# Performance work log

Hardware: AMD Instinct MI355X
Metric: run time of the kernel (lower is better)

The kernel has to match this reference:

```python
import jax, jax.numpy as jnp
import numpy as np

D_MODEL = 1024
D_STATE = 16
EPS = 1e-5


def _layernorm(x, g, b):
    mu = x.mean(-1, keepdims=True)
    xc = x - mu
    var = (xc * xc).mean(-1, keepdims=True)
    return xc * jax.lax.rsqrt(var + EPS) * g + b


def setup_inputs() -> dict:
    key = jax.random.key(0)
    ks = jax.random.split(key, 10)
    B, L, d, n = 8, 1024, D_MODEL, D_STATE
    s = 1.0 / np.sqrt(d)
    return {
        "x": jax.random.normal(ks[0], (B, L, d), jnp.float32),
        "h_prev": jnp.zeros((B, d * n), jnp.float32),
        "ln_g": jnp.ones((d,), jnp.float32),
        "ln_b": jnp.zeros((d,), jnp.float32),
        "W_ig": jax.random.uniform(ks[1], (2 * d, d), jnp.float32, -s, s),
        "W_dt": jax.random.uniform(ks[2], (d, d), jnp.float32, -s, s),
        "b_dt": jax.random.uniform(ks[3], (d,), jnp.float32, -s, s),
        "A_log": jax.random.uniform(ks[4], (d, n), jnp.float32, -3.0, -1.0),
        "W_B": jax.random.uniform(ks[5], (n, d), jnp.float32, -s, s),
        "W_C": jax.random.uniform(ks[6], (n, d), jnp.float32, -s, s),
        "D": jnp.ones((d,), jnp.float32),
        "W_out": jax.random.uniform(ks[7], (d, d), jnp.float32, -s, s),
    }


def reference(x, h_prev, ln_g, ln_b, W_ig, W_dt, b_dt, A_log, W_B, W_C, D, W_out):
    Bsz, L, d = x.shape
    n = A_log.shape[1]
    x_norm = _layernorm(x, ln_g, ln_b)
    x_proj = jnp.einsum('bld,ed->ble', x_norm, W_ig)  # [B,L,2d]
    x_in, z = x_proj[..., :d], x_proj[..., d:]
    dt = jax.nn.softplus(jnp.einsum('bld,ed->ble', x_in, W_dt) + b_dt)  # [B,L,d]
    A = -jnp.exp(A_log)  # [d,n]
    B_t = jnp.einsum('bld,nd->bln', x_in, W_B)  # [B,L,n]
    C_t = jnp.einsum('bld,nd->bln', x_in, W_C)  # [B,L,n]
    h0 = h_prev.reshape(Bsz, d, n)

    def step(h, inp):
        dt_t, xin_t, Bt_t, Ct_t = inp  # [B,d],[B,d],[B,n],[B,n]
        dA = jnp.exp(dt_t[..., None] * A)                      # [B,d,n]
        h = dA * h + (dt_t * xin_t)[..., None] * Bt_t[:, None, :]
        y_t = (h * Ct_t[:, None, :]).sum(-1)                   # [B,d]
        return h, y_t

    xs = (jnp.swapaxes(dt, 0, 1), jnp.swapaxes(x_in, 0, 1),
          jnp.swapaxes(B_t, 0, 1), jnp.swapaxes(C_t, 0, 1))
    h_final, y = jax.lax.scan(step, h0, xs)
    y = jnp.swapaxes(y, 0, 1)  # [B,L,d]
    ssm_out = y * jax.nn.silu(z) + x_in * D
    out = jnp.einsum('bld,ed->ble', ssm_out, W_out)
    return (x + out, h_final.reshape(Bsz, -1))
```

## Files before the change

kernel.cpp:

```cpp
#include <hip/hip_runtime.h>
#include <hip/hip_bf16.h>
#include <math.h>

#define DM 1024
#define NS 16
#define BSZ 8
#define LSEQ 1024
#define MROWS (BSZ*LSEQ)
#define CH 32
#define ROWP 36

typedef __bf16 bf16;
typedef bf16 bf16x8 __attribute__((ext_vector_type(8)));
typedef bf16 bf16x4 __attribute__((ext_vector_type(4)));
typedef float f32x4 __attribute__((ext_vector_type(4)));
typedef unsigned int u32;
typedef unsigned short u16;
typedef u32 u32x4 __attribute__((ext_vector_type(4)));

__device__ __forceinline__ void async16(const void* g, void* l) {
  __builtin_amdgcn_global_load_lds((const __attribute__((address_space(1))) void*)g,
                                   (__attribute__((address_space(3))) void*)l,
                                   16, 0, 0);
}

__device__ __forceinline__ float bflo(u32 u) { return __builtin_bit_cast(float, (u32)(u << 16)); }
__device__ __forceinline__ float bfhi(u32 u) { return __builtin_bit_cast(float, (u32)(u & 0xffff0000u)); }

template <int CTRL>
__device__ __forceinline__ float dpp_shr_add(float y) {
  int s = __builtin_amdgcn_update_dpp(0, __builtin_bit_cast(int, y), CTRL, 0xf, 0xf, true);
  return y + __builtin_bit_cast(float, s);
}
__device__ __forceinline__ float row16_sum(float y) {
  y = dpp_shr_add<0x111>(y);
  y = dpp_shr_add<0x112>(y);
  y = dpp_shr_add<0x114>(y);
  y = dpp_shr_add<0x118>(y);
  return y;
}

__global__ void cast_f2b(const float* __restrict__ s, bf16* __restrict__ d, int n4) {
  int i = blockIdx.x * 256 + threadIdx.x;
  if (i < n4) {
    float4 v = ((const float4*)s)[i];
    bf16x4 o;
    o.x = (bf16)v.x; o.y = (bf16)v.y; o.z = (bf16)v.z; o.w = (bf16)v.w;
    *(bf16x4*)(d + 4 * (size_t)i) = o;
  }
}

__global__ void transpose_cast(const float* __restrict__ src, bf16* __restrict__ dst) {
  __shared__ float tile[64][65];
  const int bk = blockIdx.x * 64;
  const int bd = blockIdx.y * 64;
  const int t = threadIdx.x;
  const int c4 = t & 15;
  const int r0 = t >> 4;
#pragma unroll
  for (int p = 0; p < 4; ++p) {
    int r = r0 + p * 16;
    float4 v = *(const float4*)(src + (size_t)(bd + r) * 1024 + bk + c4 * 4);
    tile[r][c4 * 4 + 0] = v.x;
    tile[r][c4 * 4 + 1] = v.y;
    tile[r][c4 * 4 + 2] = v.z;
    tile[r][c4 * 4 + 3] = v.w;
  }
  __syncthreads();
#pragma unroll
  for (int p = 0; p < 4; ++p) {
    int r = r0 + p * 16;
    bf16x4 o;
    o.x = (bf16)tile[c4 * 4 + 0][r];
    o.y = (bf16)tile[c4 * 4 + 1][r];
    o.z = (bf16)tile[c4 * 4 + 2][r];
    o.w = (bf16)tile[c4 * 4 + 3][r];
    *(bf16x4*)(dst + (size_t)(bk + r) * 1024 + bd + c4 * 4) = o;
  }
}

__global__ void ln_kernel(const float* __restrict__ x, const float* __restrict__ g,
                          const float* __restrict__ b, bf16* __restrict__ out) {
  const size_t row = blockIdx.x;
  const int t = threadIdx.x;
  float4 v = ((const float4*)(x + row * DM))[t];
  float s = v.x + v.y + v.z + v.w;
  float s2 = v.x*v.x + v.y*v.y + v.z*v.z + v.w*v.w;
#pragma unroll
  for (int m = 1; m < 64; m <<= 1) { s += __shfl_xor(s, m, 64); s2 += __shfl_xor(s2, m, 64); }
  __shared__ float red[8];
  int wave = t >> 6, lane = t & 63;
  if (lane == 0) { red[wave] = s; red[4 + wave] = s2; }
  __syncthreads();
  s  = red[0] + red[1] + red[2] + red[3];
  s2 = red[4] + red[5] + red[6] + red[7];
  float mu  = s * (1.f / DM);
  float var = s2 * (1.f / DM) - mu * mu;
  float inv = rsqrtf(var + 1e-5f);
  float4 gg = ((const float4*)g)[t];
  float4 bb = ((const float4*)b)[t];
  bf16x4 o;
  o.x = (bf16)((v.x - mu) * inv * gg.x + bb.x);
  o.y = (bf16)((v.y - mu) * inv * gg.y + bb.y);
  o.z = (bf16)((v.z - mu) * inv * gg.z + bb.z);
  o.w = (bf16)((v.w - mu) * inv * gg.w + bb.w);
  *(bf16x4*)(out + row * DM + t * 4) = o;
}

template <int EPI, bool SWZ>
__global__ __launch_bounds__(256)
void gemm_bf16(const bf16* __restrict__ A, const bf16* __restrict__ W, int K,
               float* __restrict__ out_f, bf16* __restrict__ out_b,
               u16* __restrict__ out_u1, u16* __restrict__ out_u2,
               const float* __restrict__ aux,
               float* __restrict__ out_f3, float* __restrict__ out_f4) {
  __shared__ bf16 As[3][128 * 32];
  __shared__ bf16 Bs[3][128 * 32];
  int tx, ty;
  if (SWZ) {
    int g = blockIdx.x;
    int xcd = g & 7, slot = g >> 3;
    tx = slot >> 3;
    ty = xcd * 8 + (slot & 7);
  } else {
    tx = blockIdx.x; ty = blockIdx.y;
  }
  const int tid  = threadIdx.x;
  const int wave = tid >> 6, lane = tid & 63;
  const int lr = lane & 15, quad = lane >> 4;
  const size_t arow = (size_t)ty * 128;
  const size_t brow = (size_t)tx * 128;
  f32x4 acc[4][4] = {};

  const int srl  = lane >> 2;
  const int kg   = lane & 3;
  const int srow = wave * 32 + srl;
  const int skc  = (kg ^ ((srl >> 1) & 3)) * 8;
  const bf16* ag = A + (arow + srow) * (size_t)K + skc;
  const bf16* wg = W + (brow + srow) * (size_t)K + skc;

  const int soff = wave * 32 * 32;
  const int ra   = (((wave >> 1) * 64) + lr) * 32 + ((quad ^ ((lr >> 1) & 3)) * 8);
  const int rb   = (((wave & 1)  * 64) + lr) * 32 + ((quad ^ ((lr >> 1) & 3)) * 8);

  bf16 *aw0 = &As[0][soff], *aw1 = &As[1][soff], *aw2 = &As[2][soff];
  bf16 *bw0 = &Bs[0][soff], *bw1 = &Bs[1][soff], *bw2 = &Bs[2][soff];
  const bf16 *ar0 = &As[0][ra], *ar1 = &As[1][ra], *ar2 = &As[2][ra];
  const bf16 *br0 = &Bs[0][rb], *br1 = &Bs[1][rb], *br2 = &Bs[2][rb];

  auto STAGE = [&](bf16* adst, bf16* bdst, int kk) {
    async16(ag + kk,                       adst);
    async16(ag + (size_t)16 * K + kk,      adst + 16 * 32);
    async16(wg + kk,                       bdst);
    async16(wg + (size_t)16 * K + kk,      bdst + 16 * 32);
  };
  auto COMPUTE = [&](const bf16* ap, const bf16* bp) {
    bf16x8 af[4], bfr[4];
#pragma unroll
    for (int i = 0; i < 4; ++i) af[i] = *(const bf16x8*)(ap + i * 16 * 32);
#pragma unroll
    for (int j = 0; j < 4; ++j) bfr[j] = *(const bf16x8*)(bp + j * 16 * 32);
#pragma unroll
    for (int i = 0; i < 4; ++i)
#pragma unroll
      for (int j = 0; j < 4; ++j)
        acc[i][j] = __builtin_amdgcn_mfma_f32_16x16x32_bf16(af[i], bfr[j], acc[i][j], 0, 0, 0);
  };

  STAGE(aw0, bw0, 0);
  STAGE(aw1, bw1, 32);
  asm volatile("s_waitcnt vmcnt(4)" ::: "memory");
  __builtin_amdgcn_s_barrier();

  for (int k0 = 0; k0 < K; k0 += 32) {
    const bool pf = (k0 + 64 < K);
    if (pf) STAGE(aw2, bw2, k0 + 64);
    COMPUTE(ar0, br0);
    if (pf) asm volatile("s_waitcnt vmcnt(4)" ::: "memory");
    else    asm volatile("s_waitcnt vmcnt(0)" ::: "memory");
    __builtin_amdgcn_s_barrier();
    bf16* t0;
    t0 = aw0; aw0 = aw1; aw1 = aw2; aw2 = t0;
    t0 = bw0; bw0 = bw1; bw1 = bw2; bw2 = t0;
    const bf16* t1;
    t1 = ar0; ar0 = ar1; ar1 = ar2; ar2 = t1;
    t1 = br0; br0 = br1; br1 = br2; br2 = t1;
  }

  const size_t mbase = arow + (wave >> 1) * 64;
  const size_t nbase = brow + (wave & 1) * 64;
  if (EPI == 0) {
    if (nbase < DM) {
#pragma unroll
      for (int i = 0; i < 4; ++i)
#pragma unroll
        for (int j = 0; j < 4; ++j)
#pragma unroll
          for (int r = 0; r < 4; ++r) {
            size_t m = mbase + i * 16 + quad * 4 + r;
            size_t n = nbase + j * 16 + lr;
            out_u1[m * DM + n] = __builtin_bit_cast(u16, (bf16)acc[i][j][r]);
          }
    } else if (nbase < 2 * DM) {
#pragma unroll
      for (int i = 0; i < 4; ++i)
#pragma unroll
        for (int j = 0; j < 4; ++j)
#pragma unroll
          for (int r = 0; r < 4; ++r) {
            size_t m = mbase + i * 16 + quad * 4 + r;
            size_t n = nbase - DM + j * 16 + lr;
            out_b[m * DM + n] = (bf16)acc[i][j][r];
          }
    } else if (nbase < 3 * DM) {
#pragma unroll
      for (int i = 0; i < 4; ++i)
#pragma unroll
        for (int j = 0; j < 4; ++j)
#pragma unroll
          for (int r = 0; r < 4; ++r) {
            size_t m = mbase + i * 16 + quad * 4 + r;
            size_t n = nbase - 2 * DM + j * 16 + lr;
            float tt = acc[i][j][r] + aux[n];
            float sp = (tt > 20.f) ? tt : __logf(1.f + __expf(tt));
            out_u2[m * DM + n] = __builtin_bit_cast(u16, (bf16)sp);
          }
    } else if (nbase < 3 * DM + 2 * NS) {
#pragma unroll
      for (int i = 0; i < 4; ++i)
#pragma unroll
        for (int r = 0; r < 4; ++r) {
          size_t m = mbase + i * 16 + quad * 4 + r;
          out_f3[m * NS + lr] = acc[i][0][r];
          out_f4[m * NS + lr] = acc[i][1][r];
        }
    }
  } else {
#pragma unroll
    for (int i = 0; i < 4; ++i)
#pragma unroll
      for (int j = 0; j < 4; ++j)
#pragma unroll
        for (int r = 0; r < 4; ++r) {
          size_t m = mbase + i * 16 + quad * 4 + r;
          size_t n = nbase + j * 16 + lr;
          float v = acc[i][j][r];
          if (EPI == 2) {
            out_f[m * DM + n] = v + aux[m * DM + n];
          } else {
            out_b[m * (size_t)DM + n] = (bf16)v;
          }
        }
  }
}

__global__ __launch_bounds__(256)
void scan_kernel(const u16* __restrict__ dt_b, const u16* __restrict__ xi_b,
                 const bf16* __restrict__ z_b,
                 const float* __restrict__ B_t, const float* __restrict__ C_t,
                 const float* __restrict__ A_log, const float* __restrict__ h_prev,
                 const float* __restrict__ Dvec,
                 bf16* __restrict__ ssm_out, float* __restrict__ h_final) {
  const int blk = blockIdx.x;
  const int b = blk >> 6;
  const int d0 = (blk & 63) * 16;
  const int t = threadIdx.x;
  const int n = t & 15, dl = t >> 4;
  const int d = d0 + dl;
  const float Ac2 = -__expf(A_log[d * NS + n]) * 1.44269504f;
  float h = h_prev[(size_t)b * DM * NS + (size_t)d * NS + n];

  __shared__ u32   dxs[2][16][ROWP];
  __shared__ float Bsh[2][16][ROWP];
  __shared__ float Csh[2][16][ROWP];
  __shared__ float y_s[16][ROWP];

  const size_t base_row = (size_t)b * LSEQ;
  const int l_a = t >> 4, c_a = t & 15;
  const float Dva = Dvec[d0 + c_a];

  {
    size_t ga = (base_row + l_a) * DM + d0 + c_a;
    size_t gb = (base_row + l_a + 16) * DM + d0 + c_a;
    dxs[0][c_a][l_a]      = (u32)dt_b[ga] | ((u32)xi_b[ga] << 16);
    dxs[0][c_a][l_a + 16] = (u32)dt_b[gb] | ((u32)xi_b[gb] << 16);
    size_t gB = base_row * NS;
    Bsh[0][c_a][l_a]      = B_t[gB + t];
    Csh[0][c_a][l_a]      = C_t[gB + t];
    Bsh[0][c_a][l_a + 16] = B_t[gB + t + 256];
    Csh[0][c_a][l_a + 16] = C_t[gB + t + 256];
  }
  float za = (float)z_b[(base_row + l_a) * DM + d0 + c_a];
  float zb = (float)z_b[(base_row + l_a + 16) * DM + d0 + c_a];
  __syncthreads();

  for (int c = 0; c < LSEQ / CH; ++c) {
    const int cur = c & 1, nxt = cur ^ 1;
    u32 pdxa, pdxb; float pBa, pBb, pCa, pCb, pza, pzb;
    if (c + 1 < LSEQ / CH) {
      size_t l0 = (size_t)(c + 1) * CH;
      size_t ga = (base_row + l0 + l_a) * DM + d0 + c_a;
      size_t gb = (base_row + l0 + l_a + 16) * DM + d0 + c_a;
      pdxa = (u32)dt_b[ga] | ((u32)xi_b[ga] << 16);
      pdxb = (u32)dt_b[gb] | ((u32)xi_b[gb] << 16);
      pza = (float)z_b[ga]; pzb = (float)z_b[gb];
      size_t gB = (base_row + l0) * NS;
      pBa = B_t[gB + t];       pCa = C_t[gB + t];
      pBb = B_t[gB + t + 256]; pCb = C_t[gB + t + 256];
    }
#pragma unroll
    for (int l4 = 0; l4 < CH; l4 += 4) {
      u32x4 dx4 = *(const u32x4*)&dxs[cur][dl][l4];
      f32x4 b4  = *(const f32x4*)&Bsh[cur][n][l4];
      f32x4 c4  = *(const f32x4*)&Csh[cur][n][l4];
      f32x4 ys4;
#pragma unroll
      for (int i = 0; i < 4; ++i) {
        float dtv = bflo(dx4[i]), xiv = bfhi(dx4[i]);
        float a = __builtin_amdgcn_exp2f(dtv * Ac2);
        h = fmaf(a, h, (dtv * xiv) * b4[i]);
        ys4[i] = row16_sum(h * c4[i]);
      }
      if (n == 15) *(f32x4*)&y_s[dl][l4] = ys4;
    }
    __syncthreads();
    {
      float s1 = y_s[c_a][l_a];
      float s2 = y_s[c_a][l_a + 16];
      float x1 = bfhi(dxs[cur][c_a][l_a]);
      float x2 = bfhi(dxs[cur][c_a][l_a + 16]);
      float g1 = za / (1.f + __expf(-za));
      float g2 = zb / (1.f + __expf(-zb));
      size_t l0 = (size_t)c * CH;
      ssm_out[(base_row + l0 + l_a) * DM + d0 + c_a]      = (bf16)(s1 * g1 + x1 * Dva);
      ssm_out[(base_row + l0 + l_a + 16) * DM + d0 + c_a] = (bf16)(s2 * g2 + x2 * Dva);
    }
    if (c + 1 < LSEQ / CH) {
      dxs[nxt][c_a][l_a]      = pdxa;
      dxs[nxt][c_a][l_a + 16] = pdxb;
      Bsh[nxt][c_a][l_a]      = pBa;
      Csh[nxt][c_a][l_a]      = pCa;
      Bsh[nxt][c_a][l_a + 16] = pBb;
      Csh[nxt][c_a][l_a + 16] = pCb;
      za = pza; zb = pzb;
    }
    __syncthreads();
  }
  h_final[(size_t)b * DM * NS + (size_t)d0 * NS + t] = h;
}

extern "C" void kernel_launch(void* const* d_in, const int* in_sizes, int n_in,
                              void* d_out, int out_size, void* d_ws, size_t ws_size,
                              hipStream_t stream) {
  const float* x      = (const float*)d_in[0];
  const float* h_prev = (const float*)d_in[1];
  const float* ln_g   = (const float*)d_in[2];
  const float* ln_b   = (const float*)d_in[3];
  const float* W_ig   = (const float*)d_in[4];
  const float* W_dt   = (const float*)d_in[5];
  const float* b_dt   = (const float*)d_in[6];
  const float* A_log  = (const float*)d_in[7];
  const float* W_B    = (const float*)d_in[8];
  const float* W_C    = (const float*)d_in[9];
  const float* Dvec   = (const float*)d_in[10];
  const float* W_out  = (const float*)d_in[11];

  char* ws = (char*)d_ws;
  size_t off = 0;
  auto alloc = [&](size_t bytes) -> char* {
    char* p = ws + off;
    off += (bytes + 255) & ~(size_t)255;
    return p;
  };
  bf16*  wmega_b = (bf16*)alloc((size_t)3200 * DM * 2);
  bf16*  wstack_b= (bf16*)alloc((size_t)1152 * DM * 2);
  bf16*  wigT_b  = (bf16*)alloc((size_t)DM * DM * 2);
  bf16*  wout_b  = (bf16*)alloc((size_t)DM * DM * 2);
  bf16*  xnorm_b = (bf16*)alloc((size_t)MROWS * DM * 2);
  u16*   xi_w    = (u16*)alloc((size_t)MROWS * DM * 2);
  u16*   dt_w    = (u16*)alloc((size_t)MROWS * DM * 2);
  bf16*  z_bb    = (bf16*)alloc((size_t)MROWS * DM * 2);
  bf16*  ssm_b   = (bf16*)alloc((size_t)MROWS * DM * 2);
  float* Bt      = (float*)alloc((size_t)MROWS * NS * 4);
  float* Ct      = (float*)alloc((size_t)MROWS * NS * 4);
  (void)ws_size; (void)in_sizes; (void)n_in; (void)out_size;

  float* out_main = (float*)d_out;
  float* out_h    = (float*)d_out + (size_t)MROWS * DM;

  cast_f2b<<<(2 * DM * DM / 4 + 255) / 256, 256, 0, stream>>>(W_ig, wmega_b, 2 * DM * DM / 4);
  cast_f2b<<<(DM * DM / 4 + 255) / 256, 256, 0, stream>>>(W_dt, wstack_b, DM * DM / 4);
  cast_f2b<<<(NS * DM / 4 + 255) / 256, 256, 0, stream>>>(W_B, wstack_b + (size_t)DM * DM, NS * DM / 4);
  cast_f2b<<<(NS * DM / 4 + 255) / 256, 256, 0, stream>>>(W_C, wstack_b + (size_t)(DM + NS) * DM, NS * DM / 4);
  cast_f2b<<<(DM * DM / 4 + 255) / 256, 256, 0, stream>>>(W_out, wout_b, DM * DM / 4);
  transpose_cast<<<dim3(16, 16), 256, 0, stream>>>(W_ig, wigT_b);

  ln_kernel<<<MROWS, 256, 0, stream>>>(x, ln_g, ln_b, xnorm_b);

  gemm_bf16<3, false><<<dim3(8, 9), 256, 0, stream>>>(wstack_b, wigT_b, DM,
      nullptr, wmega_b + (size_t)2048 * DM, nullptr, nullptr, nullptr, nullptr, nullptr);

  gemm_bf16<0, true><<<1600, 256, 0, stream>>>(xnorm_b, wmega_b, DM,
      nullptr, z_bb, xi_w, dt_w, b_dt, Bt, Ct);

  scan_kernel<<<512, 256, 0, stream>>>(dt_w, xi_w, z_bb, Bt, Ct, A_log, h_prev,
                                       Dvec, ssm_b, out_h);

  gemm_bf16<2, true><<<512, 256, 0, stream>>>(ssm_b, wout_b, DM,
      out_main, nullptr, nullptr, nullptr, x, nullptr, nullptr);
}
```

Before: 359.0 us.

## Store x_in, z and dt in channel-group-blocked layout for coalesced scan loads

The projection GEMM epilogue now writes x_in, z and dt as [d/16][rows][16] tiles instead of row-major [rows][d]. The scan kernel, which handles 16 channels per block, can then read each chunk as one contiguous span indexed by thread id rather than 32-byte fragments strided by DM. This targets the scattered 2-byte loads in the latency-bound scan. The GEMM stores become strided by MROWS*16, and any other consumer of these buffers, such as the output stage using x_in*D, has to use the same layout.

```diff
diff --git a/kernel.cpp b/kernel.cpp
--- a/kernel.cpp
+++ b/kernel.cpp
@@ -194,37 +194,41 @@
 #pragma unroll
       for (int i = 0; i < 4; ++i)
 #pragma unroll
-        for (int j = 0; j < 4; ++j)
+        for (int j = 0; j < 4; ++j) {
+          size_t gx = (nbase >> 4) + j;
 #pragma unroll
           for (int r = 0; r < 4; ++r) {
             size_t m = mbase + i * 16 + quad * 4 + r;
-            size_t n = nbase + j * 16 + lr;
-            out_u1[m * DM + n] = __builtin_bit_cast(u16, (bf16)acc[i][j][r]);
+            out_u1[(gx * (size_t)MROWS + m) * 16 + lr] = __builtin_bit_cast(u16, (bf16)acc[i][j][r]);
           }
+        }
     } else if (nbase < 2 * DM) {
 #pragma unroll
       for (int i = 0; i < 4; ++i)
 #pragma unroll
-        for (int j = 0; j < 4; ++j)
+        for (int j = 0; j < 4; ++j) {
+          size_t gz = ((nbase - DM) >> 4) + j;
 #pragma unroll
           for (int r = 0; r < 4; ++r) {
             size_t m = mbase + i * 16 + quad * 4 + r;
-            size_t n = nbase - DM + j * 16 + lr;
-            out_b[m * DM + n] = (bf16)acc[i][j][r];
+            out_b[(gz * (size_t)MROWS + m) * 16 + lr] = (bf16)acc[i][j][r];
           }
+        }
     } else if (nbase < 3 * DM) {
 #pragma unroll
       for (int i = 0; i < 4; ++i)
 #pragma unroll
-        for (int j = 0; j < 4; ++j)
+        for (int j = 0; j < 4; ++j) {
+          size_t gd = ((nbase - 2 * DM) >> 4) + j;
+          size_t nb = nbase - 2 * DM + j * 16 + lr;
 #pragma unroll
           for (int r = 0; r < 4; ++r) {
             size_t m = mbase + i * 16 + quad * 4 + r;
-            size_t n = nbase - 2 * DM + j * 16 + lr;
-            float tt = acc[i][j][r] + aux[n];
+            float tt = acc[i][j][r] + aux[nb];
             float sp = (tt > 20.f) ? tt : __logf(1.f + __expf(tt));
-            out_u2[m * DM + n] = __builtin_bit_cast(u16, (bf16)sp);
+            out_u2[(gd * (size_t)MROWS + m) * 16 + lr] = __builtin_bit_cast(u16, (bf16)sp);
           }
+        }
     } else if (nbase < 3 * DM + 2 * NS) {
 #pragma unroll
       for (int i = 0; i < 4; ++i)
@@ -263,7 +267,8 @@
                  bf16* __restrict__ ssm_out, float* __restrict__ h_final) {
   const int blk = blockIdx.x;
   const int b = blk >> 6;
-  const int d0 = (blk & 63) * 16;
+  const int g = blk & 63;
+  const int d0 = g * 16;
   const int t = threadIdx.x;
   const int n = t & 15, dl = t >> 4;
   const int d = d0 + dl;
@@ -276,35 +281,32 @@
   __shared__ float y_s[16][ROWP];
 
   const size_t base_row = (size_t)b * LSEQ;
+  const size_t base16 = ((size_t)g * MROWS + base_row) * 16;
   const int l_a = t >> 4, c_a = t & 15;
   const float Dva = Dvec[d0 + c_a];
 
   {
-    size_t ga = (base_row + l_a) * DM + d0 + c_a;
-    size_t gb = (base_row + l_a + 16) * DM + d0 + c_a;
-    dxs[0][c_a][l_a]      = (u32)dt_b[ga] | ((u32)xi_b[ga] << 16);
-    dxs[0][c_a][l_a + 16] = (u32)dt_b[gb] | ((u32)xi_b[gb] << 16);
+    dxs[0][c_a][l_a]      = (u32)dt_b[base16 + t]       | ((u32)xi_b[base16 + t] << 16);
+    dxs[0][c_a][l_a + 16] = (u32)dt_b[base16 + 256 + t] | ((u32)xi_b[base16 + 256 + t] << 16);
     size_t gB = base_row * NS;
     Bsh[0][c_a][l_a]      = B_t[gB + t];
     Csh[0][c_a][l_a]      = C_t[gB + t];
     Bsh[0][c_a][l_a + 16] = B_t[gB + t + 256];
     Csh[0][c_a][l_a + 16] = C_t[gB + t + 256];
   }
-  float za = (float)z_b[(base_row + l_a) * DM + d0 + c_a];
-  float zb = (float)z_b[(base_row + l_a + 16) * DM + d0 + c_a];
+  float za = (float)z_b[base16 + t];
+  float zb = (float)z_b[base16 + 256 + t];
   __syncthreads();
 
   for (int c = 0; c < LSEQ / CH; ++c) {
     const int cur = c & 1, nxt = cur ^ 1;
     u32 pdxa, pdxb; float pBa, pBb, pCa, pCb, pza, pzb;
     if (c + 1 < LSEQ / CH) {
-      size_t l0 = (size_t)(c + 1) * CH;
-      size_t ga = (base_row + l0 + l_a) * DM + d0 + c_a;
-      size_t gb = (base_row + l0 + l_a + 16) * DM + d0 + c_a;
-      pdxa = (u32)dt_b[ga] | ((u32)xi_b[ga] << 16);
-      pdxb = (u32)dt_b[gb] | ((u32)xi_b[gb] << 16);
-      pza = (float)z_b[ga]; pzb = (float)z_b[gb];
-      size_t gB = (base_row + l0) * NS;
+      size_t off = base16 + (size_t)(c + 1) * (CH * 16);
+      pdxa = (u32)dt_b[off + t]       | ((u32)xi_b[off + t] << 16);
+      pdxb = (u32)dt_b[off + 256 + t] | ((u32)xi_b[off + 256 + t] << 16);
+      pza = (float)z_b[off + t]; pzb = (float)z_b[off + 256 + t];
+      size_t gB = (base_row + (size_t)(c + 1) * CH) * NS;
       pBa = B_t[gB + t];       pCa = C_t[gB + t];
       pBb = B_t[gB + t + 256]; pCb = C_t[gB + t + 256];
     }
```

New measurement: 366.3 us. 1.02x slower.
